# Kernel optimization log

Measured on AMD Instinct MI355X. Metric: run time of the kernel, lower is better.

## Reference

```python
import jax, jax.numpy as jnp
import numpy as np
from jax import lax

N_QUBITS = 12
N_LAYERS = 5
DIM = 2 ** N_QUBITS
EPS = 1e-5


def _linear(x, W, b):
    return x @ W.T + b


def _bn(x, g, b):
    # BatchNorm1d in training mode: biased batch statistics
    mu = jnp.mean(x, axis=0)
    var = jnp.var(x, axis=0)
    return g * (x - mu) * lax.rsqrt(var + EPS) + b


def _leaky(x):
    return jax.nn.leaky_relu(x, 0.01)


def _gate_matrices(w):
    # w: (L, Q, 3) -> composite U3 @ RZ @ RY @ RX per (layer, qubit): (L, Q, 2, 2) complex64
    a, b, c = w[..., 0], w[..., 1], w[..., 2]
    ca = jnp.cos(a / 2).astype(jnp.complex64)
    sa = jnp.sin(a / 2).astype(jnp.complex64)
    cb = jnp.cos(b / 2).astype(jnp.complex64)
    sb = jnp.sin(b / 2).astype(jnp.complex64)
    zero = jnp.zeros_like(ca)

    def mat(m00, m01, m10, m11):
        return jnp.stack([jnp.stack([m00, m01], -1), jnp.stack([m10, m11], -1)], -2)

    RX = mat(ca, -1j * sa, -1j * sa, ca)
    RY = mat(cb, -sb, sb, cb)
    ez = jnp.exp(-0.5j * c.astype(jnp.complex64))
    RZ = mat(ez, zero, zero, jnp.conj(ez))
    eip = jnp.exp(1j * b.astype(jnp.complex64))
    eid = jnp.exp(1j * c.astype(jnp.complex64))
    U3 = mat(ca, -eid * sa, eip * sa, eip * eid * ca)  # pennylane U3(theta=a, phi=b, delta=c)
    mm = lambda A, B: jnp.einsum('lqab,lqbc->lqac', A, B)
    return mm(U3, mm(RZ, mm(RY, RX)))


def _apply1q(state, U, w):
    # state: (B, 2, ..., 2); U: (2, 2) shared across batch
    s = jnp.moveaxis(state, 1 + w, -1)
    s = jnp.einsum('...a,ca->...c', s, U)
    return jnp.moveaxis(s, -1, 1 + w)


def _cnot(state, c, t):
    s = jnp.moveaxis(state, (1 + c, 1 + t), (-2, -1))
    s = jnp.stack([s[..., 0, :], s[..., 1, ::-1]], axis=-2)
    return jnp.moveaxis(s, (-2, -1), (1 + c, 1 + t))


def _quantum(x_pre, qw):
    # Batched statevector simulation of the pennylane circuit. x_pre: (B, 12)
    B = x_pre.shape[0]
    half = x_pre * (jnp.pi / 2)  # RY(x*pi) from |0> -> [cos(x*pi/2), sin(x*pi/2)]
    vec = jnp.stack([jnp.cos(half), jnp.sin(half)], axis=-1).astype(jnp.complex64)  # (B, Q, 2)
    state = vec[:, 0]
    for q in range(1, N_QUBITS):
        state = jnp.einsum('b...,bq->b...q', state, vec[:, q])  # (B, 2, ..., 2)
    G = _gate_matrices(qw)
    for l in range(N_LAYERS):
        for q in range(N_QUBITS):
            state = _apply1q(state, G[l, q], q)
        if l % 2 == 0:
            for q in range(N_QUBITS - 1):
                state = _cnot(state, q, q + 1)
            state = _cnot(state, N_QUBITS - 1, 0)
        else:
            for q in range(0, N_QUBITS, 2):
                state = _cnot(state, q, (q + N_QUBITS // 2) % N_QUBITS)
    probs = jnp.abs(state.reshape(B, DIM)) ** 2
    idx = np.arange(DIM)
    bits = (idx[None, :] >> (N_QUBITS - 1 - np.arange(N_QUBITS))[:, None]) & 1  # (Q, DIM)
    zsigns = jnp.asarray(1.0 - 2.0 * bits, dtype=jnp.float32)
    zvals = probs @ zsigns.T  # (B, Q) PauliZ expectations
    xvals = []
    for q in range(N_QUBITS // 2):  # PauliX expectations on first Q/2 wires
        s = jnp.moveaxis(state, 1 + q, -1).reshape(B, DIM // 2, 2)
        xvals.append(2.0 * jnp.sum(jnp.real(jnp.conj(s[..., 0]) * s[..., 1]), axis=1))
    return jnp.concatenate([zvals, jnp.stack(xvals, axis=1)], axis=1)  # (B, 18)


def setup_inputs():
    key = jax.random.key(0)
    ks = jax.random.split(key, 16)
    B, NF = 4096, 64

    def W(k, o, i):
        return jax.random.normal(k, (o, i), jnp.float32) * (1.0 / np.sqrt(i))

    z = lambda n: jnp.zeros((n,), jnp.float32)
    o = lambda n: jnp.ones((n,), jnp.float32)
    return {
        'x': jax.random.normal(ks[0], (B, NF), jnp.float32),
        'Ws': W(ks[1], 128, NF), 'bs': z(128),
        'W1': W(ks[2], 256, NF), 'b1': z(256), 'g1': o(256), 'be1': z(256),
        'W2': W(ks[3], 128, 256), 'b2': z(128), 'g2': o(128), 'be2': z(128),
        'W3': W(ks[4], 64, 128), 'b3': z(64), 'g3': o(64), 'be3': z(64),
        'Wp': W(ks[5], N_QUBITS, 64), 'bp': z(N_QUBITS),
        'qw': jax.random.normal(ks[6], (N_LAYERS, N_QUBITS, 3), jnp.float32) * 0.1,
        'Wq1': W(ks[7], 128, 18), 'bq1': z(128), 'gq1': o(128), 'beq1': z(128),
        'Wq2': W(ks[8], 64, 128), 'bq2': z(64), 'gq2': o(64), 'beq2': z(64),
        'Wo1': W(ks[9], 32, 64), 'bo1': z(32),
        'Wo2': W(ks[10], 1, 32), 'bo2': z(1),
    }


def reference(x, Ws, bs, W1, b1, g1, be1, W2, b2, g2, be2, W3, b3, g3, be3,
              Wp, bp, qw, Wq1, bq1, gq1, beq1, Wq2, bq2, gq2, beq2,
              Wo1, bo1, Wo2, bo2):
    skip = _linear(x, Ws, bs)
    x1 = _leaky(_bn(_linear(x, W1, b1), g1, be1))          # dropout is eval-mode identity
    x2 = _leaky(_bn(_linear(x1, W2, b2), g2, be2))
    x3 = _leaky(_bn(_linear(x2, W3, b3), g3, be3)) + 0.1 * x1[:, :64]
    x_pre = jnp.tanh(_linear(x3, Wp, bp))
    q_out = lax.stop_gradient(_quantum(x_pre, qw))         # torch detaches the quantum path
    p1 = _leaky(_bn(_linear(q_out, Wq1, bq1), gq1, beq1)) + skip
    p2 = _leaky(_bn(_linear(p1, Wq2, bq2), gq2, beq2))
    return _linear(_leaky(_linear(p2, Wo1, bo1)), Wo2, bo2)  # (B, 1)
```

## Files before the change

kernel.cpp:

```cpp
#include <hip/hip_runtime.h>
#include <math.h>

#define LEAKY(v) ((v) > 0.f ? (v) : 0.01f * (v))

typedef float f2v __attribute__((ext_vector_type(2)));

__device__ __forceinline__ void cmm2(const float* Ar, const float* Ai,
                                     const float* Br, const float* Bi,
                                     float* Cr, float* Ci) {
#pragma unroll
  for (int r = 0; r < 2; r++)
#pragma unroll
    for (int c = 0; c < 2; c++) {
      float xr = 0.f, xi = 0.f;
#pragma unroll
      for (int k = 0; k < 2; k++) {
        float ar = Ar[r*2+k], ai = Ai[r*2+k];
        float br = Br[k*2+c], bi = Bi[k*2+c];
        xr += ar*br - ai*bi;
        xi += ar*bi + ai*br;
      }
      Cr[r*2+c] = xr; Ci[r*2+c] = xi;
    }
}

__global__ __launch_bounds__(256) void prep_k(const float* __restrict__ qw,
                                              float* __restrict__ gates,
                                              float* __restrict__ stats) {
  int t = threadIdx.x;
  for (int i = t; i < 1280; i += 256) stats[i] = 0.f;
  if (t < 60) {
    float a = qw[t*3+0], b = qw[t*3+1], c = qw[t*3+2];
    float ca = cosf(0.5f*a), sa = sinf(0.5f*a);
    float cb = cosf(0.5f*b), sb = sinf(0.5f*b);
    float RXr[4] = {ca, 0.f, 0.f, ca};
    float RXi[4] = {0.f, -sa, -sa, 0.f};
    float RYr[4] = {cb, -sb, sb, cb};
    float RYi[4] = {0.f, 0.f, 0.f, 0.f};
    float hc = 0.5f*c;
    float RZr[4] = {cosf(hc), 0.f, 0.f, cosf(hc)};
    float RZi[4] = {-sinf(hc), 0.f, 0.f, sinf(hc)};
    float epr = cosf(b), epi = sinf(b);
    float edr = cosf(c), edi = sinf(c);
    float eer = epr*edr - epi*edi, eei = epr*edi + epi*edr;
    float U3r[4] = {ca, -edr*sa, epr*sa, eer*ca};
    float U3i[4] = {0.f, -edi*sa, epi*sa, eei*ca};
    float T1r[4],T1i[4],T2r[4],T2i[4],Gr[4],Gi[4];
    cmm2(RYr,RYi, RXr,RXi, T1r,T1i);
    cmm2(RZr,RZi, T1r,T1i, T2r,T2i);
    cmm2(U3r,U3i, T2r,T2i, Gr,Gi);
#pragma unroll
    for (int m = 0; m < 4; m++) {
      gates[t*8 + 2*m]     = Gr[m];
      gates[t*8 + 2*m + 1] = Gi[m];
    }
  }
}

struct GemmLds {
  float As[32][65];
  float Bs[64][65];
  float sc1[256], sh1[256];
  float sc2[128], sh2[128];
};

__device__ __forceinline__ void load_chunk(
    int tid, int r0, int c0, int kc, int K, int N,
    const float* __restrict__ A1, int ld1,
    const float* __restrict__ A2, int ld2, float scale2,
    bool lk1, bool lk2, const float* __restrict__ W,
    const float* sc1, const float* sh1,
    const float* sc2, const float* sh2,
    float* pa, float* pw) {
#pragma unroll
  for (int i = 0; i < 8; i++) {
    int t = tid + 256*i;
    int lr = t >> 6, lk = t & 63;
    int k = kc + lk;
    float av = 0.f;
    if (k < K) {
      float v1 = A1[(size_t)(r0+lr)*ld1 + k];
      v1 = sc1[k]*v1 + sh1[k];
      if (lk1) v1 = LEAKY(v1);
      av = v1;
      if (A2) {
        float v2 = A2[(size_t)(r0+lr)*ld2 + k];
        v2 = sc2[k]*v2 + sh2[k];
        if (lk2) v2 = LEAKY(v2);
        av += scale2 * v2;
      }
    }
    pa[i] = av;
  }
#pragma unroll
  for (int i = 0; i < 16; i++) {
    int t = tid + 256*i;
    int lr = t >> 6, lk = t & 63;
    int k = kc + lk;
    float wv = 0.f;
    if (k < K && c0 + lr < N) wv = W[(size_t)(c0+lr)*K + k];
    pw[i] = wv;
  }
}

__device__ __forceinline__ void gemm_body(
    GemmLds& L, int bx, int by,
    const float* __restrict__ A1, const float* __restrict__ st1,
    const float* __restrict__ g1, const float* __restrict__ be1, int ld1,
    const float* __restrict__ A2, const float* __restrict__ st2,
    const float* __restrict__ g2, const float* __restrict__ be2, int ld2,
    float scale2,
    const float* __restrict__ W, const float* __restrict__ bias,
    float* __restrict__ C, float* __restrict__ statsOut, int N, int K) {
  const int r0 = bx * 32;
  const int c0 = by * 64;
  const int tid = threadIdx.x;
  const int ty = tid >> 4, tx = tid & 15;
  const bool lk1 = (st1 != nullptr);
  const bool lk2 = (st2 != nullptr);
  for (int k = tid; k < K; k += 256) {
    if (lk1) {
      float mean = st1[2*k] * (1.f/4096.f);
      float var  = st1[2*k+1] * (1.f/4096.f) - mean*mean;
      float s = g1[k] * rsqrtf(var + 1e-5f);
      L.sc1[k] = s; L.sh1[k] = be1[k] - mean*s;
    } else { L.sc1[k] = 1.f; L.sh1[k] = 0.f; }
    if (A2 && k < 128) {
      if (lk2) {
        float mean = st2[2*k] * (1.f/4096.f);
        float var  = st2[2*k+1] * (1.f/4096.f) - mean*mean;
        float s = g2[k] * rsqrtf(var + 1e-5f);
        L.sc2[k] = s; L.sh2[k] = be2[k] - mean*s;
      } else { L.sc2[k] = 1.f; L.sh2[k] = 0.f; }
    }
  }
  __syncthreads();
  float acc[2][4] = {};
  float pa[8], pw[16];
  load_chunk(tid, r0, c0, 0, K, N, A1, ld1, A2, ld2, scale2,
             lk1, lk2, W, L.sc1, L.sh1, L.sc2, L.sh2, pa, pw);
  for (int kc = 0; kc < K; kc += 64) {
#pragma unroll
    for (int i = 0; i < 8; i++)  { int t = tid + 256*i; L.As[t>>6][t&63] = pa[i]; }
#pragma unroll
    for (int i = 0; i < 16; i++) { int t = tid + 256*i; L.Bs[t>>6][t&63] = pw[i]; }
    __syncthreads();
    if (kc + 64 < K)
      load_chunk(tid, r0, c0, kc + 64, K, N, A1, ld1, A2, ld2, scale2,
                 lk1, lk2, W, L.sc1, L.sh1, L.sc2, L.sh2, pa, pw);
#pragma unroll 16
    for (int kk = 0; kk < 64; kk++) {
      float ar[2], wr[4];
      ar[0] = L.As[ty*2][kk];
      ar[1] = L.As[ty*2+1][kk];
#pragma unroll
      for (int j = 0; j < 4; j++) wr[j] = L.Bs[tx*4+j][kk];
#pragma unroll
      for (int i = 0; i < 2; i++)
#pragma unroll
        for (int j = 0; j < 4; j++)
          acc[i][j] = fmaf(ar[i], wr[j], acc[i][j]);
    }
    __syncthreads();
  }
  float bv[4];
#pragma unroll
  for (int j = 0; j < 4; j++) {
    int c = c0 + tx*4 + j;
    bv[j] = (c < N) ? bias[c] : 0.f;
  }
#pragma unroll
  for (int i = 0; i < 2; i++) {
    int r = r0 + ty*2 + i;
#pragma unroll
    for (int j = 0; j < 4; j++) {
      int c = c0 + tx*4 + j;
      if (c < N) C[(size_t)r*N + c] = acc[i][j] + bv[j];
    }
  }
  if (statsOut) {
#pragma unroll
    for (int j = 0; j < 4; j++) {
      float s = 0.f, q = 0.f;
#pragma unroll
      for (int i = 0; i < 2; i++) {
        float v = acc[i][j] + bv[j];
        s += v; q += v*v;
      }
      L.As[ty][tx*4+j] = s;
      L.Bs[ty][tx*4+j] = q;
    }
    __syncthreads();
    if (tid < 64) {
      float s = 0.f, q = 0.f;
#pragma unroll
      for (int t = 0; t < 16; t++) { s += L.As[t][tid]; q += L.Bs[t][tid]; }
      int c = c0 + tid;
      if (c < N) {
        atomicAdd(&statsOut[2*c], s);
        atomicAdd(&statsOut[2*c+1], q);
      }
    }
  }
}

__global__ __launch_bounds__(256) void gemm_f(
    const float* __restrict__ A1, const float* __restrict__ st1,
    const float* __restrict__ g1, const float* __restrict__ be1, int ld1,
    const float* __restrict__ A2, const float* __restrict__ st2,
    const float* __restrict__ g2, const float* __restrict__ be2, int ld2,
    float scale2,
    const float* __restrict__ W, const float* __restrict__ bias,
    float* __restrict__ C, float* __restrict__ statsOut, int N, int K) {
  __shared__ GemmLds L;
  gemm_body(L, blockIdx.x, blockIdx.y, A1, st1, g1, be1, ld1,
            A2, st2, g2, be2, ld2, scale2, W, bias, C, statsOut, N, K);
}

__global__ __launch_bounds__(256) void z1skip_k(
    const float* __restrict__ x,
    const float* __restrict__ W1, const float* __restrict__ b1,
    float* __restrict__ BUF1, float* __restrict__ ST1,
    const float* __restrict__ Wsk, const float* __restrict__ bs,
    float* __restrict__ SKIP) {
  __shared__ GemmLds L;
  if (blockIdx.y < 4)
    gemm_body(L, blockIdx.x, blockIdx.y, x, nullptr,nullptr,nullptr, 64,
              nullptr,nullptr,nullptr,nullptr, 0, 0.f,
              W1, b1, BUF1, ST1, 256, 64);
  else
    gemm_body(L, blockIdx.x, blockIdx.y - 4, x, nullptr,nullptr,nullptr, 64,
              nullptr,nullptr,nullptr,nullptr, 0, 0.f,
              Wsk, bs, SKIP, nullptr, 128, 64);
}

__device__ __forceinline__ int SWZi(int i) { return i ^ ((i >> 4) & 15); }
__device__ __forceinline__ int LINV_E(int i) {
  return i ^ ((i >> 1) & 0x7FF) ^ ((i & 1) ? 0xC00 : 0);
}
__device__ __forceinline__ int LINV_O(int i) {
  int hi = i & 0xAAA;
  return (i & 0x555) | ((hi ^ (hi << 6)) & 0xA80) | ((hi >> 6) & 0x2A);
}

template<int B>
__device__ __forceinline__ void gate16(f2v* a, const float* __restrict__ g) {
  const float g00r=g[0], g00i=g[1], g01r=g[2], g01i=g[3];
  const float g10r=g[4], g10i=g[5], g11r=g[6], g11i=g[7];
#pragma unroll
  for (int m = 0; m < 8; m++) {
    const int l0 = ((m >> B) << (B+1)) | (m & ((1<<B)-1));
    const int l1 = l0 | (1 << B);
    f2v A = a[l0], Bv = a[l1];
    f2v Ai; Ai.x = -A.y;  Ai.y = A.x;
    f2v Bi; Bi.x = -Bv.y; Bi.y = Bv.x;
    a[l0] = g00r*A + (g00i*Ai + (g01r*Bv + g01i*Bi));
    a[l1] = g10r*A + (g10i*Ai + (g11r*Bv + g11i*Bi));
  }
}

__global__ __launch_bounds__(256, 4) void quantum_k(
    const float* __restrict__ z3buf,
    const float* __restrict__ z1buf,
    const float* __restrict__ stats,
    const float* __restrict__ g1, const float* __restrict__ be1,
    const float* __restrict__ g3, const float* __restrict__ be3,
    const float* __restrict__ Wp, const float* __restrict__ bp,
    const float* __restrict__ gates,
    float* __restrict__ qout) {
  __shared__ f2v st[4096];
  float* stf = (float*)st;
  const int tid = threadIdx.x, b = blockIdx.x;
  if (tid < 64) {
    const float* ST3 = stats + 768;
    float mean = ST3[2*tid] * (1.f/4096.f);
    float var  = ST3[2*tid+1] * (1.f/4096.f) - mean*mean;
    float s = g3[tid] * rsqrtf(var + 1e-5f);
    stf[tid] = s; stf[64+tid] = be3[tid] - mean*s;
  } else if (tid < 128) {
    int k = tid - 64;
    float mean = stats[2*k] * (1.f/4096.f);
    float var  = stats[2*k+1] * (1.f/4096.f) - mean*mean;
    float s = g1[k] * rsqrtf(var + 1e-5f);
    stf[128+k] = s; stf[192+k] = be1[k] - mean*s;
  }
  __syncthreads();
  if (tid < 64) {
    int k = tid;
    float v3 = stf[k]*z3buf[(size_t)b*64 + k] + stf[64+k];
    v3 = LEAKY(v3);
    float v1 = stf[128+k]*z1buf[(size_t)b*256 + k] + stf[192+k];
    v1 = LEAKY(v1);
    stf[256+k] = v3 + 0.1f*v1;
  }
  __syncthreads();
  if (tid < 12) {
    float acc = bp[tid];
#pragma unroll 8
    for (int k = 0; k < 64; k++) acc = fmaf(stf[256+k], Wp[tid*64+k], acc);
    float xp = tanhf(acc);
    float h = xp * 1.57079632679489662f;
    stf[320+tid] = cosf(h);
    stf[332+tid] = sinf(h);
  }
  __syncthreads();
  float cs[12], sn[12];
#pragma unroll
  for (int q = 0; q < 12; q++) { cs[q] = stf[320+q]; sn[q] = stf[332+q]; }
  __syncthreads();
  f2v a[16];
  {
    float pre = 1.f;
#pragma unroll
    for (int q = 0; q < 8; q++) pre *= ((tid >> (7-q)) & 1) ? sn[q] : cs[q];
#pragma unroll
    for (int l = 0; l < 16; l++) {
      float v = pre;
      v *= (l & 8) ? sn[8]  : cs[8];
      v *= (l & 4) ? sn[9]  : cs[9];
      v *= (l & 2) ? sn[10] : cs[10];
      v *= (l & 1) ? sn[11] : cs[11];
      a[l].x = v; a[l].y = 0.f;
    }
  }
  const int mA    = tid & 15;
  const int baseA = (tid << 4) | mA;
  const int baseB = ((tid >> 4) << 8) | mA;
  const int baseC = tid ^ ((tid >> 4) & 15);
  const int gE    = SWZi(LINV_E(tid << 4));
  const int gO    = SWZi(LINV_O(tid << 4));
  for (int layer = 0; layer < 5; layer++) {
    const float* gl = gates + layer * 96;
    gate16<3>(a, gl + 64); gate16<2>(a, gl + 72);
    gate16<1>(a, gl + 80); gate16<0>(a, gl + 88);
#pragma unroll
    for (int l = 0; l < 16; l++) st[baseA ^ l] = a[l];
    __syncthreads();
#pragma unroll
    for (int l = 0; l < 16; l++) a[l] = st[baseB ^ ((l << 4) | l)];
    gate16<3>(a, gl + 32); gate16<2>(a, gl + 40);
    gate16<1>(a, gl + 48); gate16<0>(a, gl + 56);
#pragma unroll
    for (int l = 0; l < 16; l++) st[baseB ^ ((l << 4) | l)] = a[l];
    __syncthreads();
#pragma unroll
    for (int l = 0; l < 16; l++) a[l] = st[baseC ^ (l << 8)];
    gate16<3>(a, gl +  0); gate16<2>(a, gl +  8);
    gate16<1>(a, gl + 16); gate16<0>(a, gl + 24);
#pragma unroll
    for (int l = 0; l < 16; l++) st[baseC ^ (l << 8)] = a[l];
    __syncthreads();
    if ((layer & 1) == 0) {
#pragma unroll
      for (int l = 0; l < 16; l++) a[l] = st[gE ^ SWZi(LINV_E(l))];
    } else {
#pragma unroll
      for (int l = 0; l < 16; l++) a[l] = st[gO ^ SWZi(LINV_O(l))];
    }
    __syncthreads();
  }
#pragma unroll
  for (int l = 0; l < 16; l++) st[baseA ^ l] = a[l];
  __syncthreads();
  float pl[16], tot = 0.f;
#pragma unroll
  for (int l = 0; l < 16; l++) { pl[l] = a[l].x*a[l].x + a[l].y*a[l].y; tot += pl[l]; }
  float part[18];
#pragma unroll
  for (int q = 0; q < 8; q++) part[q] = ((tid >> (7-q)) & 1) ? -tot : tot;
#pragma unroll
  for (int q = 8; q < 12; q++) {
    const int bit = 11 - q;
    float s = 0.f;
#pragma unroll
    for (int l = 0; l < 16; l++) s += ((l >> bit) & 1) ? -pl[l] : pl[l];
    part[q] = s;
  }
#pragma unroll
  for (int q = 0; q < 6; q++) {
    const int bt = 7 - q;
    float s = 0.f;
    if (((tid >> bt) & 1) == 0) {
      const int tid2 = tid | (1 << bt);
      const int baseA2 = (tid2 << 4) | (tid2 & 15);
#pragma unroll
      for (int l = 0; l < 16; l++) {
        f2v bb = st[baseA2 ^ l];
        s += a[l].x*bb.x + a[l].y*bb.y;
      }
    }
    part[12+q] = 2.f * s;
  }
  __syncthreads();
#pragma unroll
  for (int j = 0; j < 18; j++) {
    float v = part[j];
#pragma unroll
    for (int m = 1; m < 64; m <<= 1) v += __shfl_xor(v, m);
    if ((tid & 63) == 0) stf[(tid >> 6)*18 + j] = v;
  }
  __syncthreads();
  if (tid < 18) qout[b*18 + tid] = stf[tid] + stf[18+tid] + stf[36+tid] + stf[54+tid];
}

__global__ __launch_bounds__(256) void final_k(const float* __restrict__ P2,
                                               const float* __restrict__ stats,
                                               const float* __restrict__ g,
                                               const float* __restrict__ be,
                                               const float* __restrict__ Wo1,
                                               const float* __restrict__ bo1,
                                               const float* __restrict__ Wo2,
                                               const float* __restrict__ bo2,
                                               float* __restrict__ out) {
  __shared__ float sc[64], sh[64];
  int tid = threadIdx.x;
  if (tid < 64) {
    float mean = stats[2*tid] * (1.f/4096.f);
    float var  = stats[2*tid+1] * (1.f/4096.f) - mean*mean;
    float s = g[tid] * rsqrtf(var + 1e-5f);
    sc[tid] = s; sh[tid] = be[tid] - mean*s;
  }
  __syncthreads();
  int row = blockIdx.x*8 + (tid >> 5);
  int o = tid & 31;
  float acc = 0.f;
#pragma unroll 8
  for (int k = 0; k < 64; k++) {
    float v = sc[k]*P2[(size_t)row*64 + k] + sh[k];
    v = LEAKY(v);
    acc = fmaf(v, Wo1[o*64 + k], acc);
  }
  float h = acc + bo1[o];
  h = LEAKY(h);
  float v = h * Wo2[o];
#pragma unroll
  for (int m = 1; m < 32; m <<= 1) v += __shfl_xor(v, m);
  if (o == 0) out[row] = v + bo2[0];
}

extern "C" void kernel_launch(void* const* d_in, const int* in_sizes, int n_in,
                              void* d_out, int out_size, void* d_ws, size_t ws_size,
                              hipStream_t stream) {
  (void)in_sizes; (void)n_in; (void)out_size; (void)ws_size;
  const float* x   = (const float*)d_in[0];
  const float* Wsk = (const float*)d_in[1];
  const float* bs  = (const float*)d_in[2];
  const float* W1  = (const float*)d_in[3];
  const float* b1  = (const float*)d_in[4];
  const float* g1  = (const float*)d_in[5];
  const float* be1 = (const float*)d_in[6];
  const float* W2  = (const float*)d_in[7];
  const float* b2  = (const float*)d_in[8];
  const float* g2  = (const float*)d_in[9];
  const float* be2 = (const float*)d_in[10];
  const float* W3  = (const float*)d_in[11];
  const float* b3  = (const float*)d_in[12];
  const float* g3  = (const float*)d_in[13];
  const float* be3 = (const float*)d_in[14];
  const float* Wp  = (const float*)d_in[15];
  const float* bp  = (const float*)d_in[16];
  const float* qw  = (const float*)d_in[17];
  const float* Wq1 = (const float*)d_in[18];
  const float* bq1 = (const float*)d_in[19];
  const float* gq1 = (const float*)d_in[20];
  const float* beq1= (const float*)d_in[21];
  const float* Wq2 = (const float*)d_in[22];
  const float* bq2 = (const float*)d_in[23];
  const float* gq2 = (const float*)d_in[24];
  const float* beq2= (const float*)d_in[25];
  const float* Wo1 = (const float*)d_in[26];
  const float* bo1 = (const float*)d_in[27];
  const float* Wo2 = (const float*)d_in[28];
  const float* bo2 = (const float*)d_in[29];
  float* out = (float*)d_out;
  float* ws = (float*)d_ws;

  float* GATES = ws;
  float* STATS = ws + 480;
  float* ST1 = STATS;
  float* ST2 = STATS + 512;
  float* ST3 = STATS + 768;
  float* SQ1 = STATS + 896;
  float* SQ2 = STATS + 1152;
  float* SKIP = ws + 2048;
  float* BUF1 = SKIP + 4096*128;
  float* BUF2 = BUF1 + 4096*256;
  float* BUF3 = BUF2 + 4096*128;
  float* QOUT = BUF3 + 4096*64 + 4096*12;

  dim3 blk(256);
  prep_k<<<1, blk, 0, stream>>>(qw, GATES, STATS);
  z1skip_k<<<dim3(128,6), blk, 0, stream>>>(x, W1, b1, BUF1, ST1, Wsk, bs, SKIP);
  gemm_f<<<dim3(128,2), blk, 0, stream>>>(BUF1, ST1, g1, be1, 256,
      nullptr,nullptr,nullptr,nullptr, 0, 0.f, W2, b2, BUF2, ST2, 128, 256);
  gemm_f<<<dim3(128,1), blk, 0, stream>>>(BUF2, ST2, g2, be2, 128,
      nullptr,nullptr,nullptr,nullptr, 0, 0.f, W3, b3, BUF3, ST3, 64, 128);
  quantum_k<<<dim3(4096), blk, 0, stream>>>(BUF3, BUF1, STATS,
      g1, be1, g3, be3, Wp, bp, GATES, QOUT);
  gemm_f<<<dim3(128,2), blk, 0, stream>>>(QOUT, nullptr,nullptr,nullptr, 18,
      nullptr,nullptr,nullptr,nullptr, 0, 0.f, Wq1, bq1, BUF2, SQ1, 128, 18);
  gemm_f<<<dim3(128,1), blk, 0, stream>>>(BUF2, SQ1, gq1, beq1, 128,
      SKIP, nullptr, nullptr, nullptr, 128, 1.0f, Wq2, bq2, BUF3, SQ2, 64, 128);
  final_k<<<dim3(512), blk, 0, stream>>>(BUF3, SQ2, gq2, beq2, Wo1, bo1, Wo2, bo2, out);
}
```

Measured before the change: 427.0 us.

## Fuse Wq1 projection into quantum kernel with sharded BN stat atomics

```diff
diff --git a/kernel.cpp b/kernel.cpp
--- a/kernel.cpp
+++ b/kernel.cpp
@@ -28,7 +28,7 @@
                                               float* __restrict__ gates,
                                               float* __restrict__ stats) {
   int t = threadIdx.x;
-  for (int i = t; i < 1280; i += 256) stats[i] = 0.f;
+  for (int i = t; i < 17408; i += 256) stats[i] = 0.f;
   if (t < 60) {
     float a = qw[t*3+0], b = qw[t*3+1], c = qw[t*3+2];
     float ca = cosf(0.5f*a), sa = sinf(0.5f*a);
@@ -107,6 +107,7 @@
     GemmLds& L, int bx, int by,
     const float* __restrict__ A1, const float* __restrict__ st1,
     const float* __restrict__ g1, const float* __restrict__ be1, int ld1,
+    int nCop1, int cstr1,
     const float* __restrict__ A2, const float* __restrict__ st2,
     const float* __restrict__ g2, const float* __restrict__ be2, int ld2,
     float scale2,
@@ -120,8 +121,16 @@
   const bool lk2 = (st2 != nullptr);
   for (int k = tid; k < K; k += 256) {
     if (lk1) {
-      float mean = st1[2*k] * (1.f/4096.f);
-      float var  = st1[2*k+1] * (1.f/4096.f) - mean*mean;
+      float sum, sq;
+      if (nCop1 > 1) {
+        sum = 0.f; sq = 0.f;
+        for (int c = 0; c < nCop1; c++) {
+          sum += st1[(size_t)c*cstr1 + 2*k];
+          sq  += st1[(size_t)c*cstr1 + 2*k + 1];
+        }
+      } else { sum = st1[2*k]; sq = st1[2*k+1]; }
+      float mean = sum * (1.f/4096.f);
+      float var  = sq * (1.f/4096.f) - mean*mean;
       float s = g1[k] * rsqrtf(var + 1e-5f);
       L.sc1[k] = s; L.sh1[k] = be1[k] - mean*s;
     } else { L.sc1[k] = 1.f; L.sh1[k] = 0.f; }
@@ -207,13 +216,14 @@
 __global__ __launch_bounds__(256) void gemm_f(
     const float* __restrict__ A1, const float* __restrict__ st1,
     const float* __restrict__ g1, const float* __restrict__ be1, int ld1,
+    int nCop1, int cstr1,
     const float* __restrict__ A2, const float* __restrict__ st2,
     const float* __restrict__ g2, const float* __restrict__ be2, int ld2,
     float scale2,
     const float* __restrict__ W, const float* __restrict__ bias,
     float* __restrict__ C, float* __restrict__ statsOut, int N, int K) {
   __shared__ GemmLds L;
-  gemm_body(L, blockIdx.x, blockIdx.y, A1, st1, g1, be1, ld1,
+  gemm_body(L, blockIdx.x, blockIdx.y, A1, st1, g1, be1, ld1, nCop1, cstr1,
             A2, st2, g2, be2, ld2, scale2, W, bias, C, statsOut, N, K);
 }
 
@@ -225,11 +235,11 @@
     float* __restrict__ SKIP) {
   __shared__ GemmLds L;
   if (blockIdx.y < 4)
-    gemm_body(L, blockIdx.x, blockIdx.y, x, nullptr,nullptr,nullptr, 64,
+    gemm_body(L, blockIdx.x, blockIdx.y, x, nullptr,nullptr,nullptr, 64, 1, 0,
               nullptr,nullptr,nullptr,nullptr, 0, 0.f,
               W1, b1, BUF1, ST1, 256, 64);
   else
-    gemm_body(L, blockIdx.x, blockIdx.y - 4, x, nullptr,nullptr,nullptr, 64,
+    gemm_body(L, blockIdx.x, blockIdx.y - 4, x, nullptr,nullptr,nullptr, 64, 1, 0,
               nullptr,nullptr,nullptr,nullptr, 0, 0.f,
               Wsk, bs, SKIP, nullptr, 128, 64);
 }
@@ -267,7 +277,9 @@
     const float* __restrict__ g3, const float* __restrict__ be3,
     const float* __restrict__ Wp, const float* __restrict__ bp,
     const float* __restrict__ gates,
-    float* __restrict__ qout) {
+    const float* __restrict__ Wq1, const float* __restrict__ bq1,
+    float* __restrict__ zq1,
+    float* __restrict__ sq1s) {
   __shared__ f2v st[4096];
   float* stf = (float*)st;
   const int tid = threadIdx.x, b = blockIdx.x;
@@ -294,14 +306,20 @@
     stf[256+k] = v3 + 0.1f*v1;
   }
   __syncthreads();
-  if (tid < 12) {
-    float acc = bp[tid];
-#pragma unroll 8
-    for (int k = 0; k < 64; k++) acc = fmaf(stf[256+k], Wp[tid*64+k], acc);
-    float xp = tanhf(acc);
-    float h = xp * 1.57079632679489662f;
-    stf[320+tid] = cosf(h);
-    stf[332+tid] = sinf(h);
+  {
+    int w = tid >> 6, lane = tid & 63;
+    float xv = stf[256 + lane];
+    for (int j = w; j < 12; j += 4) {
+      float v = xv * Wp[j*64 + lane];
+#pragma unroll
+      for (int m = 1; m < 64; m <<= 1) v += __shfl_xor(v, m);
+      if (lane == 0) {
+        float xp = tanhf(v + bp[j]);
+        float h = xp * 1.57079632679489662f;
+        stf[320+j] = cosf(h);
+        stf[332+j] = sinf(h);
+      }
+    }
   }
   __syncthreads();
   float cs[12], sn[12];
@@ -400,7 +418,17 @@
     if ((tid & 63) == 0) stf[(tid >> 6)*18 + j] = v;
   }
   __syncthreads();
-  if (tid < 18) qout[b*18 + tid] = stf[tid] + stf[18+tid] + stf[36+tid] + stf[54+tid];
+  if (tid < 18) stf[72+tid] = stf[tid] + stf[18+tid] + stf[36+tid] + stf[54+tid];
+  __syncthreads();
+  if (tid < 128) {
+    float acc = bq1[tid];
+#pragma unroll
+    for (int k = 0; k < 18; k++) acc = fmaf(stf[72+k], Wq1[tid*18+k], acc);
+    zq1[(size_t)b*128 + tid] = acc;
+    float* slot = sq1s + (b & 63) * 256;
+    atomicAdd(&slot[2*tid], acc);
+    atomicAdd(&slot[2*tid+1], acc*acc);
+  }
 }
 
 __global__ __launch_bounds__(256) void final_k(const float* __restrict__ P2,
@@ -477,29 +505,27 @@
 
   float* GATES = ws;
   float* STATS = ws + 480;
-  float* ST1 = STATS;
-  float* ST2 = STATS + 512;
-  float* ST3 = STATS + 768;
-  float* SQ1 = STATS + 896;
-  float* SQ2 = STATS + 1152;
-  float* SKIP = ws + 2048;
+  float* ST1  = STATS;
+  float* ST2  = STATS + 512;
+  float* ST3  = STATS + 768;
+  float* SQ2  = STATS + 896;
+  float* SQ1S = STATS + 1024;
+  float* SKIP = ws + 18432;
   float* BUF1 = SKIP + 4096*128;
   float* BUF2 = BUF1 + 4096*256;
   float* BUF3 = BUF2 + 4096*128;
-  float* QOUT = BUF3 + 4096*64 + 4096*12;
+  (void)ST3;
 
   dim3 blk(256);
   prep_k<<<1, blk, 0, stream>>>(qw, GATES, STATS);
   z1skip_k<<<dim3(128,6), blk, 0, stream>>>(x, W1, b1, BUF1, ST1, Wsk, bs, SKIP);
-  gemm_f<<<dim3(128,2), blk, 0, stream>>>(BUF1, ST1, g1, be1, 256,
+  gemm_f<<<dim3(128,2), blk, 0, stream>>>(BUF1, ST1, g1, be1, 256, 1, 0,
       nullptr,nullptr,nullptr,nullptr, 0, 0.f, W2, b2, BUF2, ST2, 128, 256);
-  gemm_f<<<dim3(128,1), blk, 0, stream>>>(BUF2, ST2, g2, be2, 128,
-      nullptr,nullptr,nullptr,nullptr, 0, 0.f, W3, b3, BUF3, ST3, 64, 128);
+  gemm_f<<<dim3(128,1), blk, 0, stream>>>(BUF2, ST2, g2, be2, 128, 1, 0,
+      nullptr,nullptr,nullptr,nullptr, 0, 0.f, W3, b3, BUF3, STATS + 768, 64, 128);
   quantum_k<<<dim3(4096), blk, 0, stream>>>(BUF3, BUF1, STATS,
-      g1, be1, g3, be3, Wp, bp, GATES, QOUT);
-  gemm_f<<<dim3(128,2), blk, 0, stream>>>(QOUT, nullptr,nullptr,nullptr, 18,
-      nullptr,nullptr,nullptr,nullptr, 0, 0.f, Wq1, bq1, BUF2, SQ1, 128, 18);
-  gemm_f<<<dim3(128,1), blk, 0, stream>>>(BUF2, SQ1, gq1, beq1, 128,
+      g1, be1, g3, be3, Wp, bp, GATES, Wq1, bq1, BUF2, SQ1S);
+  gemm_f<<<dim3(128,1), blk, 0, stream>>>(BUF2, SQ1S, gq1, beq1, 128, 64, 256,
       SKIP, nullptr, nullptr, nullptr, 128, 1.0f, Wq2, bq2, BUF3, SQ2, 64, 128);
   final_k<<<dim3(512), blk, 0, stream>>>(BUF3, SQ2, gq2, beq2, Wo1, bo1, Wo2, bo2, out);
 }
```

Result: slower. 436.3 us (+2.2%).
